# Optimization experiments

Measured on AMD Instinct MI355X. Metric: run time of the kernel, lower is better.

Reference implementation:

```python
import jax, jax.numpy as jnp
import numpy as np

BS, D, N, E, L, NE = 8, 512, 2048, 8, 64, 524288


def conv1d_same(x, w, b):
    # x: [B, W, Cin], w: [K, Cin, Cout] -> [B, W, Cout], stride 1, 'same' padding
    y = jax.lax.conv_general_dilated(x, w, window_strides=(1,), padding='SAME',
                                     dimension_numbers=('NWC', 'WIO', 'NWC'))
    return y + b


def setup_inputs() -> dict:
    key = jax.random.key(0)
    ks = jax.random.split(key, 10)
    def nrm(k, shape, s=1.0):
        return jax.random.normal(k, shape, jnp.float32) * s
    return {
        'latent': nrm(ks[0], (BS, D)),
        'edge_index': jax.random.randint(ks[1], (2, NE), 0, BS * N),
        'W_dense': nrm(ks[2], (D, N), 0.05),
        'b_dense': jnp.zeros((N,), jnp.float32),
        'conv1_w': nrm(ks[3], (3, 1, E), 0.3),
        'conv1_b': jnp.zeros((E,), jnp.float32),
        'gat_Wq': nrm(ks[4], (E, E), 0.3),
        'gat_bq': jnp.zeros((E,), jnp.float32),
        'gat_Wk': nrm(ks[5], (E, E), 0.3),
        'gat_bk': jnp.zeros((E,), jnp.float32),
        'gat_Wv': nrm(ks[6], (E, E), 0.3),
        'gat_bias': jnp.zeros((E,), jnp.float32),
        'qkv_w': nrm(ks[7], (3, E, 3 * E * L), 0.1),
        'qkv_b': jnp.zeros((3 * E * L,), jnp.float32),
    }


def reference(latent, edge_index, W_dense, b_dense, conv1_w, conv1_b,
              gat_Wq, gat_bq, gat_Wk, gat_bk, gat_Wv, gat_bias, qkv_w, qkv_b):
    bs = latent.shape[0]
    # Dense -> [bs, N], expand -> Conv1D(E) -> [bs, N, E]
    skeleton = latent @ W_dense + b_dense
    skeleton = conv1d_same(skeleton[..., None], conv1_w, conv1_b)
    # concat(unstack, axis=0) == reshape to batched graph nodes [bs*N, E]
    x = skeleton.reshape(bs * N, E)
    BN = bs * N
    # GAT (tf_geometric, num_heads=1): add self-loops, per-edge dot-attention,
    # segment softmax over destination (row), scatter-sum aggregate.
    loops = jnp.arange(BN)
    row = jnp.concatenate([edge_index[0], loops])
    col = jnp.concatenate([edge_index[1], loops])
    Q = jax.nn.leaky_relu(x @ gat_Wq + gat_bq, 0.2)
    K = jax.nn.leaky_relu(x @ gat_Wk + gat_bk, 0.2)
    V = x @ gat_Wv
    score = jnp.sum(Q[row] * K[col], axis=-1)            # [n_edges + BN]
    smax = jax.ops.segment_max(score, row, num_segments=BN)
    ex = jnp.exp(score - smax[row])
    ssum = jax.ops.segment_sum(ex, row, num_segments=BN)
    alpha = ex / ssum[row]                               # segment softmax
    h = jax.ops.segment_sum(alpha[:, None] * V[col], row, num_segments=BN) + gat_bias
    graph = h.reshape(bs, N, E)                          # stack(split(., bs))
    # QVK conv over node axis -> [bs, N, 3*E*L]
    qvk = conv1d_same(graph, qkv_w, qkv_b)
    # stack(split(., L, -1), 1) then concat(unstack(., -2), -1)
    qvk = qvk.reshape(bs, N, L, 3 * E).transpose(0, 2, 1, 3).reshape(bs, L, N * 3 * E)
    q, v, k = jnp.split(qvk, 3, axis=-1)                 # each [bs, L, N*E]
    # keras Attention (use_scale=False): softmax(q @ k^T) @ v
    attn = jax.nn.softmax(jnp.einsum('btd,bsd->bts', q, k), axis=-1)
    seq = jnp.einsum('bts,bsd->btd', attn, v)
    # stack(split(., N, -1), -2) == reshape [bs, L, N, E]
    return seq.reshape(bs, L, N, E)
```

## Files before the change

kernel.cpp:

```cpp
#include <hip/hip_runtime.h>
#include <hip/hip_bf16.h>
#include <math.h>

#define BSZ 8
#define DDIM 512
#define NND 2048
#define EE 8
#define LLH 64
#define NEDGE 524288
#define BNN 16384
#define OCC 1536
#define DQ 16384

typedef __attribute__((ext_vector_type(8))) short short8;
typedef __attribute__((ext_vector_type(4))) unsigned short ushort4v;

__device__ inline unsigned short f2bf(float x) {
    __hip_bfloat16 h = __float2bfloat16(x);
    return __builtin_bit_cast(unsigned short, h);
}
__device__ inline float bf2f(unsigned short u) {
    return __uint_as_float(((unsigned int)u) << 16);
}

__global__ __launch_bounds__(256) void k_densep(const float* __restrict__ latent,
                                                const float* __restrict__ Wd,
                                                const float* __restrict__ qw,
                                                const float* __restrict__ qb,
                                                float* __restrict__ pdense,
                                                int* __restrict__ hist,
                                                float* __restrict__ BsT) {
    int n0 = blockIdx.x * 32, d0 = blockIdx.y * 64;
    __shared__ float lat[8][64];
    int tid = threadIdx.x;
    if (blockIdx.y == 0) hist[blockIdx.x * 256 + tid] = 0;
    if (blockIdx.y == 1) {
        for (int idx = blockIdx.x * 256 + tid; idx < 38400; idx += 16384) {
            int jc = idx >> 6, s = idx & 63;
            int j = jc / 24, c = jc - j * 24;
            int sc = (c < 16) ? c + 8 : c - 16;
            BsT[idx] = (j < 24) ? qw[(size_t)j * OCC + s * 24 + sc] : qb[s * 24 + sc];
        }
    }
    #pragma unroll
    for (int r = 0; r < 2; ++r) {
        int i = r * 256 + tid;
        lat[i >> 6][i & 63] = latent[(i >> 6) * DDIM + d0 + (i & 63)];
    }
    __syncthreads();
    int nl = tid & 31, b = tid >> 5;
    const float* wp = Wd + (size_t)d0 * NND + n0 + nl;
    float acc = 0.f;
    #pragma unroll 8
    for (int d = 0; d < 64; ++d) acc += lat[b][d] * wp[(size_t)d * NND];
    pdense[((size_t)blockIdx.y * BSZ + b) * NND + n0 + nl] = acc;
}

__global__ __launch_bounds__(256) void k_gat(const float* __restrict__ pdense,
                                             const float* __restrict__ bd,
                                             const float* __restrict__ w1,
                                             const float* __restrict__ b1,
                                             const float* __restrict__ Wq, const float* __restrict__ bq,
                                             const float* __restrict__ Wk, const float* __restrict__ bk,
                                             const float* __restrict__ Wv,
                                             const int* __restrict__ ei,
                                             float* __restrict__ Qg, float* __restrict__ Kg,
                                             float* __restrict__ Vg, int* __restrict__ hist) {
    int gid = blockIdx.x * 256 + threadIdx.x;
    int i = gid >> 3, j = gid & 7;
    int b = i >> 11, n = i & (NND - 1);
    float sm = 0.f, s0 = 0.f, sp = 0.f;
    #pragma unroll
    for (int ds = 0; ds < 8; ++ds) {
        const float* p = pdense + ((size_t)ds * BSZ + b) * NND + n;
        if (n > 0) sm += p[-1];
        s0 += p[0];
        if (n < NND - 1) sp += p[1];
    }
    if (n > 0) sm += bd[n - 1];
    s0 += bd[n];
    if (n < NND - 1) sp += bd[n + 1];
    float q = bq[j], k = bk[j], v = 0.f;
    #pragma unroll
    for (int c = 0; c < EE; ++c) {
        float xc = sm * w1[c] + s0 * w1[EE + c] + sp * w1[2 * EE + c] + b1[c];
        q += xc * Wq[c * EE + j];
        k += xc * Wk[c * EE + j];
        v += xc * Wv[c * EE + j];
    }
    Qg[(size_t)i * EE + j] = (q >= 0.f) ? q : 0.2f * q;
    Kg[(size_t)i * EE + j] = (k >= 0.f) ? k : 0.2f * k;
    Vg[(size_t)i * EE + j] = v;
    #pragma unroll
    for (int r = 0; r < 4; ++r)
        atomicAdd(hist + ei[gid + r * 131072], 1);
}

__global__ __launch_bounds__(1024) void k_scan(const int* __restrict__ hist,
                                               int* __restrict__ offs,
                                               int* __restrict__ cnt) {
    int tid = threadIdx.x;
    int lane = tid & 63, wv = tid >> 6;
    const int4* hp = (const int4*)(hist + tid * 16);
    int4 a = hp[0], b4 = hp[1], c4 = hp[2], d4 = hp[3];
    int h[16] = {a.x, a.y, a.z, a.w, b4.x, b4.y, b4.z, b4.w,
                 c4.x, c4.y, c4.z, c4.w, d4.x, d4.y, d4.z, d4.w};
    int mysum = 0;
    #pragma unroll
    for (int i = 0; i < 16; ++i) mysum += h[i];
    int inc = mysum;
    #pragma unroll
    for (int off = 1; off < 64; off <<= 1) {
        int u = __shfl_up(inc, off, 64);
        if (lane >= off) inc += u;
    }
    __shared__ int wtot[16];
    if (lane == 63) wtot[wv] = inc;
    __syncthreads();
    if (tid < 16) {
        int t = wtot[tid];
        #pragma unroll
        for (int off = 1; off < 16; off <<= 1) {
            int u = __shfl_up(t, off, 16);
            if (tid >= off) t += u;
        }
        wtot[tid] = t;
    }
    __syncthreads();
    int run = (wv ? wtot[wv - 1] : 0) + inc - mysum;
    #pragma unroll
    for (int i = 0; i < 16; ++i) {
        offs[tid * 16 + i] = run;
        cnt[tid * 16 + i] = run;
        run += h[i];
    }
}

__global__ void k_scatter(const int* __restrict__ ei, int* __restrict__ cnt,
                          int* __restrict__ ecol) {
    int e = blockIdx.x * 256 + threadIdx.x;
    if (e >= NEDGE) return;
    int r = ei[e], c = ei[NEDGE + e];
    int pos = atomicAdd(cnt + r, 1);
    ecol[pos] = c;
}

__global__ __launch_bounds__(256) void k_gatagg(const int* __restrict__ ecol,
                                                const int* __restrict__ offs,
                                                const int* __restrict__ hist,
                                                const float* __restrict__ Qg,
                                                const float* __restrict__ Kg,
                                                const float* __restrict__ Vg,
                                                const float* __restrict__ gbias,
                                                float* __restrict__ hg) {
    int row = __builtin_amdgcn_readfirstlane(blockIdx.x * 4 + (threadIdx.x >> 6));
    int lane = threadIdx.x & 63;
    const float* Qr = Qg + (size_t)row * EE;
    float q0 = Qr[0], q1 = Qr[1], q2 = Qr[2], q3 = Qr[3];
    float q4 = Qr[4], q5 = Qr[5], q6 = Qr[6], q7 = Qr[7];
    int beg = offs[row], deg = hist[row];
    int total = deg + 1;
    float m = -INFINITY, l = 0.f;
    float acc[EE];
    #pragma unroll
    for (int j = 0; j < EE; ++j) acc[j] = 0.f;
    for (int base = 0; base < total; base += 64) {
        int idx = base + lane;
        int c = row;
        if (idx < deg) c = ecol[beg + idx];
        const float4* K4 = (const float4*)(Kg + (size_t)c * EE);
        float4 ka = K4[0], kb = K4[1];
        float s = q0*ka.x + q1*ka.y + q2*ka.z + q3*ka.w
                + q4*kb.x + q5*kb.y + q6*kb.z + q7*kb.w;
        if (idx >= total) s = -INFINITY;
        float pm = s;
        #pragma unroll
        for (int off = 32; off > 0; off >>= 1) pm = fmaxf(pm, __shfl_xor(pm, off));
        float nm = fmaxf(m, pm);
        float scale = __expf(m - nm);
        float p = (idx < total) ? __expf(s - nm) : 0.f;
        float ps = p;
        #pragma unroll
        for (int off = 32; off > 0; off >>= 1) ps += __shfl_xor(ps, off);
        l = l * scale + ps;
        const float4* V4 = (const float4*)(Vg + (size_t)c * EE);
        float4 va = V4[0], vb = V4[1];
        float pv[EE] = {p*va.x, p*va.y, p*va.z, p*va.w, p*vb.x, p*vb.y, p*vb.z, p*vb.w};
        #pragma unroll
        for (int j = 0; j < EE; ++j) {
            float t = pv[j];
            #pragma unroll
            for (int off = 32; off > 0; off >>= 1) t += __shfl_xor(t, off);
            acc[j] = acc[j] * scale + t;
        }
        m = nm;
    }
    if (lane < EE)
        hg[(size_t)row * EE + lane] = acc[lane] / l + gbias[lane];
}

__global__ __launch_bounds__(256) void k_convV(const float* __restrict__ hg,
                                               const float* __restrict__ qw,
                                               const float* __restrict__ qb,
                                               unsigned short* __restrict__ FvT,
                                               float* __restrict__ Mpart) {
    int bx = blockIdx.x, b = blockIdx.y, tid = threadIdx.x;
    if (bx < 86) {
        int n0 = 682 + bx * 8;
        __shared__ float hs[10 * EE];
        __shared__ unsigned short st[8 * 768];
        for (int i = tid; i < 10 * EE; i += 256) {
            int nn = n0 - 1 + (i >> 3);
            hs[i] = (nn < NND) ? hg[((size_t)b * NND + nn) * EE + (i & 7)] : 0.f;
        }
        __syncthreads();
        int dbase = n0 * 24 - DQ;
        #pragma unroll
        for (int pass = 0; pass < 2; ++pass) {
            if (pass) __syncthreads();
            float w[3][24], bias[3];
            #pragma unroll
            for (int rr = 0; rr < 3; ++rr) {
                int o = pass * 768 + rr * 256 + tid;
                bias[rr] = qb[o];
                #pragma unroll
                for (int kk = 0; kk < 24; ++kk) w[rr][kk] = qw[kk * OCC + o];
            }
            #pragma unroll
            for (int nn = 0; nn < 8; ++nn) {
                const float* hv = &hs[nn * EE];
                float a0 = bias[0], a1 = bias[1], a2 = bias[2];
                #pragma unroll
                for (int kk = 0; kk < 24; ++kk) {
                    float h = hv[kk];
                    a0 += h * w[0][kk]; a1 += h * w[1][kk]; a2 += h * w[2][kk];
                }
                st[nn * 768 + tid]       = f2bf(a0);
                st[nn * 768 + tid + 256] = f2bf(a1);
                st[nn * 768 + tid + 512] = f2bf(a2);
            }
            __syncthreads();
            int l0 = pass * 32;
            #pragma unroll
            for (int it = 0; it < 6; ++it) {
                int idx = it * 256 + tid;
                int dl = idx >> 3, s4 = idx & 7;
                int d = dbase + dl;
                if (d < 0 || d >= DQ) continue;
                int nn = dl / 24, c = dl - nn * 24;
                const unsigned short* sb = st + nn * 768 + c;
                ushort4v v4 = { sb[(s4 * 4 + 0) * 24], sb[(s4 * 4 + 1) * 24],
                                sb[(s4 * 4 + 2) * 24], sb[(s4 * 4 + 3) * 24] };
                *(ushort4v*)(FvT + ((size_t)b * DQ + d) * 64 + l0 + s4 * 4) = v4;
            }
        }
    } else {
        int sp = bx - 86;
        int nq0 = sp * 86;
        __shared__ float hq[88 * EE];
        __shared__ float hk[90 * EE];
        for (int i = tid; i < 88 * EE; i += 256) {
            int r = nq0 - 1 + (i >> 3);
            hq[i] = (r >= 0 && r < NND) ? hg[((size_t)b * NND + r) * EE + (i & 7)] : 0.f;
        }
        for (int i = tid; i < 90 * EE; i += 256) {
            int r = nq0 + 1364 + (i >> 3);
            hk[i] = (r < NND) ? hg[((size_t)b * NND + r) * EE + (i & 7)] : 0.f;
        }
        __syncthreads();
        int cnt1 = 683 - nq0; if (cnt1 > 86) cnt1 = 86; if (cnt1 < 0) cnt1 = 0;
        int cnt2 = 682 - nq0; if (cnt2 > 86) cnt2 = 86; if (cnt2 < 0) cnt2 = 0;
        for (int idx = tid; idx < 1250; idx += 256) {
            int mm = idx / 625, p = idx - (idx / 625) * 625;
            int i = p / 25, j = p - (p / 25) * 25;
            int cnt = mm ? cnt2 : cnt1;
            int qi = i >> 3, qe = i & 7;
            int kj = (j >> 3) + mm, ke = j & 7;
            float acc = 0.f;
            if (i < 24 && j < 24) {
                for (int nl = 0; nl < cnt; ++nl)
                    acc += hq[(nl + qi) * EE + qe] * hk[(nl + kj) * EE + ke];
            } else if (i < 24) {
                for (int nl = 0; nl < cnt; ++nl) acc += hq[(nl + qi) * EE + qe];
            } else if (j < 24) {
                for (int nl = 0; nl < cnt; ++nl) acc += hk[(nl + kj) * EE + ke];
            } else {
                acc = (float)cnt;
            }
            Mpart[((size_t)(sp * 8 + b)) * 1250 + idx] = acc;
        }
    }
}

__global__ __launch_bounds__(256) void k_Ssm(const float* __restrict__ qw,
                                             const float* __restrict__ qb,
                                             const float* __restrict__ Mpart,
                                             const float* __restrict__ BsT,
                                             float* __restrict__ atT) {
    int t = blockIdx.x, b = blockIdx.y, tid = threadIdx.x;
    __shared__ float Ms[1250];
    __shared__ float As[600];
    __shared__ float T1[600];
    __shared__ float part[4][64];
    for (int idx = tid; idx < 1250; idx += 256) {
        float s = 0.f;
        #pragma unroll
        for (int sp = 0; sp < 8; ++sp)
            s += Mpart[((size_t)(sp * 8 + b)) * 1250 + idx];
        Ms[idx] = s;
    }
    for (int idx = tid; idx < 600; idx += 256) {
        int i = idx / 24, c = idx - (idx / 24) * 24;
        As[idx] = (i < 24) ? qw[(size_t)i * OCC + t * 24 + c] : qb[t * 24 + c];
    }
    __syncthreads();
    for (int idx = tid; idx < 600; idx += 256) {
        int j = idx / 24, c = idx - (idx / 24) * 24;
        int mo = (c < 16) ? 0 : 625;
        float acc = 0.f;
        #pragma unroll 5
        for (int i = 0; i < 25; ++i)
            acc += Ms[mo + i * 25 + j] * As[i * 24 + c];
        T1[idx] = acc;
    }
    __syncthreads();
    int s = tid & 63, g = tid >> 6;
    float acc = 0.f;
    const float* bp = BsT + (size_t)(g * 150) * 64 + s;
    #pragma unroll 10
    for (int u = 0; u < 150; ++u)
        acc += T1[g * 150 + u] * bp[(size_t)u * 64];
    part[g][s] = acc;
    __syncthreads();
    if (tid < 64) {
        float v = part[0][s] + part[1][s] + part[2][s] + part[3][s];
        float m = v;
        #pragma unroll
        for (int off = 32; off > 0; off >>= 1) m = fmaxf(m, __shfl_xor(m, off));
        float e = __expf(v - m);
        float sum = e;
        #pragma unroll
        for (int off = 32; off > 0; off >>= 1) sum += __shfl_xor(sum, off);
        atT[((size_t)b * LLH + s) * LLH + t] = e / sum;
    }
}

__global__ __launch_bounds__(256) void k_attnV(const unsigned short* __restrict__ FvT,
                                               const float* __restrict__ atT,
                                               float* __restrict__ out) {
    int b = blockIdx.y;
    int d0 = blockIdx.x * 64;
    int tid = threadIdx.x;
    __shared__ float vtf[64][65];
    #pragma unroll
    for (int r = 0; r < 2; ++r) {
        int idx = r * 256 + tid;
        int dl = idx >> 3, g = idx & 7;
        short8 v = *(const short8*)(FvT + ((size_t)b * DQ + d0 + dl) * 64 + g * 8);
        #pragma unroll
        for (int j = 0; j < 8; ++j)
            vtf[dl][g * 8 + j] = bf2f((unsigned short)v[j]);
    }
    __syncthreads();
    int lane = tid & 63;
    int t0 = __builtin_amdgcn_readfirstlane((tid >> 6) * 16);
    const float* arow = atT + (size_t)b * LLH * LLH + t0;
    float acc[16];
    #pragma unroll
    for (int tt = 0; tt < 16; ++tt) acc[tt] = 0.f;
    #pragma unroll 4
    for (int s = 0; s < LLH; ++s) {
        float vv = vtf[lane][s];
        #pragma unroll
        for (int tt = 0; tt < 16; ++tt)
            acc[tt] += arow[s * LLH + tt] * vv;
    }
    float* ob = out + ((size_t)b * LLH + t0) * DQ + d0 + lane;
    #pragma unroll
    for (int tt = 0; tt < 16; ++tt) ob[(size_t)tt * DQ] = acc[tt];
}

extern "C" void kernel_launch(void* const* d_in, const int* in_sizes, int n_in,
                              void* d_out, int out_size, void* d_ws, size_t ws_size,
                              hipStream_t stream) {
    (void)in_sizes; (void)n_in; (void)out_size; (void)ws_size;
    const float* latent = (const float*)d_in[0];
    const int*   ei     = (const int*)d_in[1];
    const float* Wd     = (const float*)d_in[2];
    const float* bd     = (const float*)d_in[3];
    const float* w1     = (const float*)d_in[4];
    const float* b1     = (const float*)d_in[5];
    const float* Wq     = (const float*)d_in[6];
    const float* bq     = (const float*)d_in[7];
    const float* Wk     = (const float*)d_in[8];
    const float* bk     = (const float*)d_in[9];
    const float* Wv     = (const float*)d_in[10];
    const float* gbias  = (const float*)d_in[11];
    const float* qw     = (const float*)d_in[12];
    const float* qb     = (const float*)d_in[13];
    float* out = (float*)d_out;

    float* ws     = (float*)d_ws;
    float* pdense = ws;
    float* Qg     = pdense + 64 * NND;
    float* Kg     = Qg + BNN * EE;
    float* Vg     = Kg + BNN * EE;
    float* hg     = Vg + BNN * EE;
    int*   hist   = (int*)(hg + BNN * EE);
    int*   offs   = hist + BNN;
    int*   cnt    = offs + BNN;
    int*   ecol   = cnt + BNN;
    float* Mp     = (float*)(ecol + NEDGE);
    float* BsT    = Mp + 80000;
    float* atT    = BsT + 38400;
    unsigned short* FvT = (unsigned short*)(atT + BSZ * LLH * LLH);

    k_densep<<<dim3(64, 8), dim3(256), 0, stream>>>(latent, Wd, qw, qb, pdense, hist, BsT);
    k_gat<<<dim3(512), dim3(256), 0, stream>>>(pdense, bd, w1, b1, Wq, bq, Wk, bk, Wv,
                                               ei, Qg, Kg, Vg, hist);
    k_scan<<<dim3(1), dim3(1024), 0, stream>>>(hist, offs, cnt);
    k_scatter<<<dim3(NEDGE / 256), dim3(256), 0, stream>>>(ei, cnt, ecol);
    k_gatagg<<<dim3(BNN / 4), dim3(256), 0, stream>>>(ecol, offs, hist,
                                                      Qg, Kg, Vg, gbias, hg);
    k_convV<<<dim3(94, 8), dim3(256), 0, stream>>>(hg, qw, qb, FvT, Mp);
    k_Ssm<<<dim3(64, 8), dim3(256), 0, stream>>>(qw, qb, Mp, BsT, atT);
    k_attnV<<<dim3(256, 8), dim3(256), 0, stream>>>(FvT, atT, out);
}
```

Before: 134.9 us.

## Merge GAT build, scan, scatter and conv/softmax stages using software grid barriers

Fuses the GAT projection, histogram scan and edge scatter into one kernel separated by atomic-counter grid barriers, and likewise fuses the conv/V kernel with the attention-score softmax kernel. The aim is to remove kernel launch gaps and idle tails between small dependent stages (eight launches become five). It relies on all 512 or 752 blocks being co-resident for the spin barriers to avoid deadlock. It also serializes the scan into a single block while the other blocks spin.

```diff
diff --git a/kernel.cpp b/kernel.cpp
--- a/kernel.cpp
+++ b/kernel.cpp
@@ -23,17 +23,32 @@
     return __uint_as_float(((unsigned int)u) << 16);
 }
 
+__device__ inline void gridbar(int* c, int target) {
+    __syncthreads();
+    if (threadIdx.x == 0) {
+        __threadfence();
+        atomicAdd(c, 1);
+        while (atomicAdd(c, 0) < target) __builtin_amdgcn_s_sleep(8);
+        __threadfence();
+    }
+    __syncthreads();
+}
+
 __global__ __launch_bounds__(256) void k_densep(const float* __restrict__ latent,
                                                 const float* __restrict__ Wd,
                                                 const float* __restrict__ qw,
                                                 const float* __restrict__ qb,
                                                 float* __restrict__ pdense,
                                                 int* __restrict__ hist,
-                                                float* __restrict__ BsT) {
+                                                float* __restrict__ BsT,
+                                                int* __restrict__ cbar) {
     int n0 = blockIdx.x * 32, d0 = blockIdx.y * 64;
     __shared__ float lat[8][64];
     int tid = threadIdx.x;
-    if (blockIdx.y == 0) hist[blockIdx.x * 256 + tid] = 0;
+    if (blockIdx.y == 0) {
+        hist[blockIdx.x * 256 + tid] = 0;
+        if (blockIdx.x == 0 && tid < 16) cbar[tid] = 0;
+    }
     if (blockIdx.y == 1) {
         for (int idx = blockIdx.x * 256 + tid; idx < 38400; idx += 16384) {
             int jc = idx >> 6, s = idx & 63;
@@ -56,93 +71,85 @@
     pdense[((size_t)blockIdx.y * BSZ + b) * NND + n0 + nl] = acc;
 }
 
-__global__ __launch_bounds__(256) void k_gat(const float* __restrict__ pdense,
-                                             const float* __restrict__ bd,
-                                             const float* __restrict__ w1,
-                                             const float* __restrict__ b1,
-                                             const float* __restrict__ Wq, const float* __restrict__ bq,
-                                             const float* __restrict__ Wk, const float* __restrict__ bk,
-                                             const float* __restrict__ Wv,
-                                             const int* __restrict__ ei,
-                                             float* __restrict__ Qg, float* __restrict__ Kg,
-                                             float* __restrict__ Vg, int* __restrict__ hist) {
-    int gid = blockIdx.x * 256 + threadIdx.x;
-    int i = gid >> 3, j = gid & 7;
-    int b = i >> 11, n = i & (NND - 1);
-    float sm = 0.f, s0 = 0.f, sp = 0.f;
-    #pragma unroll
-    for (int ds = 0; ds < 8; ++ds) {
-        const float* p = pdense + ((size_t)ds * BSZ + b) * NND + n;
-        if (n > 0) sm += p[-1];
-        s0 += p[0];
-        if (n < NND - 1) sp += p[1];
-    }
-    if (n > 0) sm += bd[n - 1];
-    s0 += bd[n];
-    if (n < NND - 1) sp += bd[n + 1];
-    float q = bq[j], k = bk[j], v = 0.f;
-    #pragma unroll
-    for (int c = 0; c < EE; ++c) {
-        float xc = sm * w1[c] + s0 * w1[EE + c] + sp * w1[2 * EE + c] + b1[c];
-        q += xc * Wq[c * EE + j];
-        k += xc * Wk[c * EE + j];
-        v += xc * Wv[c * EE + j];
-    }
-    Qg[(size_t)i * EE + j] = (q >= 0.f) ? q : 0.2f * q;
-    Kg[(size_t)i * EE + j] = (k >= 0.f) ? k : 0.2f * k;
-    Vg[(size_t)i * EE + j] = v;
-    #pragma unroll
-    for (int r = 0; r < 4; ++r)
-        atomicAdd(hist + ei[gid + r * 131072], 1);
-}
-
-__global__ __launch_bounds__(1024) void k_scan(const int* __restrict__ hist,
-                                               int* __restrict__ offs,
-                                               int* __restrict__ cnt) {
+__global__ __launch_bounds__(256) void k_gatFull(const float* __restrict__ pdense,
+                                                 const float* __restrict__ bd,
+                                                 const float* __restrict__ w1,
+                                                 const float* __restrict__ b1,
+                                                 const float* __restrict__ Wq, const float* __restrict__ bq,
+                                                 const float* __restrict__ Wk, const float* __restrict__ bk,
+                                                 const float* __restrict__ Wv,
+                                                 const int* __restrict__ ei,
+                                                 float* __restrict__ Qg, float* __restrict__ Kg,
+                                                 float* __restrict__ Vg, int* __restrict__ hist,
+                                                 int* __restrict__ offs, int* __restrict__ cnt,
+                                                 int* __restrict__ ecol, int* __restrict__ cbar) {
     int tid = threadIdx.x;
-    int lane = tid & 63, wv = tid >> 6;
-    const int4* hp = (const int4*)(hist + tid * 16);
-    int4 a = hp[0], b4 = hp[1], c4 = hp[2], d4 = hp[3];
-    int h[16] = {a.x, a.y, a.z, a.w, b4.x, b4.y, b4.z, b4.w,
-                 c4.x, c4.y, c4.z, c4.w, d4.x, d4.y, d4.z, d4.w};
-    int mysum = 0;
-    #pragma unroll
-    for (int i = 0; i < 16; ++i) mysum += h[i];
-    int inc = mysum;
-    #pragma unroll
-    for (int off = 1; off < 64; off <<= 1) {
-        int u = __shfl_up(inc, off, 64);
-        if (lane >= off) inc += u;
-    }
-    __shared__ int wtot[16];
-    if (lane == 63) wtot[wv] = inc;
-    __syncthreads();
-    if (tid < 16) {
-        int t = wtot[tid];
-        #pragma unroll
-        for (int off = 1; off < 16; off <<= 1) {
-            int u = __shfl_up(t, off, 16);
-            if (tid >= off) t += u;
-        }
-        wtot[tid] = t;
-    }
-    __syncthreads();
-    int run = (wv ? wtot[wv - 1] : 0) + inc - mysum;
-    #pragma unroll
-    for (int i = 0; i < 16; ++i) {
-        offs[tid * 16 + i] = run;
-        cnt[tid * 16 + i] = run;
-        run += h[i];
-    }
-}
-
-__global__ void k_scatter(const int* __restrict__ ei, int* __restrict__ cnt,
-                          int* __restrict__ ecol) {
-    int e = blockIdx.x * 256 + threadIdx.x;
-    if (e >= NEDGE) return;
-    int r = ei[e], c = ei[NEDGE + e];
-    int pos = atomicAdd(cnt + r, 1);
-    ecol[pos] = c;
+    int gid = blockIdx.x * 256 + tid;
+    {
+        int i = gid >> 3, j = gid & 7;
+        int b = i >> 11, n = i & (NND - 1);
+        float sm = 0.f, s0 = 0.f, sp = 0.f;
+        #pragma unroll
+        for (int ds = 0; ds < 8; ++ds) {
+            const float* p = pdense + ((size_t)ds * BSZ + b) * NND + n;
+            if (n > 0) sm += p[-1];
+            s0 += p[0];
+            if (n < NND - 1) sp += p[1];
+        }
+        if (n > 0) sm += bd[n - 1];
+        s0 += bd[n];
+        if (n < NND - 1) sp += bd[n + 1];
+        float q = bq[j], k = bk[j], v = 0.f;
+        #pragma unroll
+        for (int c = 0; c < EE; ++c) {
+            float xc = sm * w1[c] + s0 * w1[EE + c] + sp * w1[2 * EE + c] + b1[c];
+            q += xc * Wq[c * EE + j];
+            k += xc * Wk[c * EE + j];
+            v += xc * Wv[c * EE + j];
+        }
+        Qg[(size_t)i * EE + j] = (q >= 0.f) ? q : 0.2f * q;
+        Kg[(size_t)i * EE + j] = (k >= 0.f) ? k : 0.2f * k;
+        Vg[(size_t)i * EE + j] = v;
+        #pragma unroll
+        for (int r = 0; r < 4; ++r)
+            atomicAdd(hist + ei[gid + r * 131072], 1);
+    }
+    gridbar(cbar + 0, 512);
+    if (blockIdx.x == 0) {
+        __shared__ int part[256];
+        int base = tid * 64;
+        const int4* h4 = (const int4*)(hist + base);
+        int sum = 0;
+        #pragma unroll
+        for (int i = 0; i < 16; ++i) { int4 v = h4[i]; sum += v.x + v.y + v.z + v.w; }
+        part[tid] = sum;
+        __syncthreads();
+        for (int off = 1; off < 256; off <<= 1) {
+            int v = (tid >= off) ? part[tid - off] : 0;
+            __syncthreads();
+            part[tid] += v;
+            __syncthreads();
+        }
+        int run = (tid > 0) ? part[tid - 1] : 0;
+        #pragma unroll
+        for (int i = 0; i < 16; ++i) {
+            int4 v = h4[i];
+            offs[base + i*4 + 0] = run; cnt[base + i*4 + 0] = run; run += v.x;
+            offs[base + i*4 + 1] = run; cnt[base + i*4 + 1] = run; run += v.y;
+            offs[base + i*4 + 2] = run; cnt[base + i*4 + 2] = run; run += v.z;
+            offs[base + i*4 + 3] = run; cnt[base + i*4 + 3] = run; run += v.w;
+        }
+    }
+    gridbar(cbar + 1, 512);
+    {
+        #pragma unroll
+        for (int r = 0; r < 4; ++r) {
+            int e = gid + r * 131072;
+            int rr = ei[e], c = ei[NEDGE + e];
+            int pos = atomicAdd(cnt + rr, 1);
+            ecol[pos] = c;
+        }
+    }
 }
 
 __global__ __launch_bounds__(256) void k_gatagg(const int* __restrict__ ecol,
@@ -199,16 +206,21 @@
         hg[(size_t)row * EE + lane] = acc[lane] / l + gbias[lane];
 }
 
-__global__ __launch_bounds__(256) void k_convV(const float* __restrict__ hg,
-                                               const float* __restrict__ qw,
-                                               const float* __restrict__ qb,
-                                               unsigned short* __restrict__ FvT,
-                                               float* __restrict__ Mpart) {
+__global__ __launch_bounds__(256) void k_convSsm(const float* __restrict__ hg,
+                                                 const float* __restrict__ qw,
+                                                 const float* __restrict__ qb,
+                                                 const float* __restrict__ Mpart_w,
+                                                 const float* __restrict__ BsT,
+                                                 unsigned short* __restrict__ FvT,
+                                                 float* __restrict__ Mpart,
+                                                 float* __restrict__ atT,
+                                                 int* __restrict__ cbar) {
+    __shared__ float smem[3456];
     int bx = blockIdx.x, b = blockIdx.y, tid = threadIdx.x;
     if (bx < 86) {
         int n0 = 682 + bx * 8;
-        __shared__ float hs[10 * EE];
-        __shared__ unsigned short st[8 * 768];
+        float* hs = smem;
+        unsigned short* st = (unsigned short*)(smem + 80);
         for (int i = tid; i < 10 * EE; i += 256) {
             int nn = n0 - 1 + (i >> 3);
             hs[i] = (nn < NND) ? hg[((size_t)b * NND + nn) * EE + (i & 7)] : 0.f;
@@ -257,8 +269,8 @@
     } else {
         int sp = bx - 86;
         int nq0 = sp * 86;
-        __shared__ float hq[88 * EE];
-        __shared__ float hk[90 * EE];
+        float* hq = smem;
+        float* hk = smem + 704;
         for (int i = tid; i < 88 * EE; i += 256) {
             int r = nq0 - 1 + (i >> 3);
             hq[i] = (r >= 0 && r < NND) ? hg[((size_t)b * NND + r) * EE + (i & 7)] : 0.f;
@@ -290,23 +302,20 @@
             Mpart[((size_t)(sp * 8 + b)) * 1250 + idx] = acc;
         }
     }
-}
-
-__global__ __launch_bounds__(256) void k_Ssm(const float* __restrict__ qw,
-                                             const float* __restrict__ qb,
-                                             const float* __restrict__ Mpart,
-                                             const float* __restrict__ BsT,
-                                             float* __restrict__ atT) {
-    int t = blockIdx.x, b = blockIdx.y, tid = threadIdx.x;
-    __shared__ float Ms[1250];
-    __shared__ float As[600];
-    __shared__ float T1[600];
-    __shared__ float part[4][64];
+    gridbar(cbar + 2, 752);
+    int fid = b * 94 + bx;
+    if (fid >= 512) return;
+    int t = fid >> 3, b2 = fid & 7;
+    float* Ms = smem;
+    float* As = smem + 1250;
+    float* T1 = smem + 1850;
+    float* part = smem + 2450;
+    __syncthreads();
     for (int idx = tid; idx < 1250; idx += 256) {
         float s = 0.f;
         #pragma unroll
         for (int sp = 0; sp < 8; ++sp)
-            s += Mpart[((size_t)(sp * 8 + b)) * 1250 + idx];
+            s += Mpart_w[((size_t)(sp * 8 + b2)) * 1250 + idx];
         Ms[idx] = s;
     }
     for (int idx = tid; idx < 600; idx += 256) {
@@ -330,10 +339,10 @@
     #pragma unroll 10
     for (int u = 0; u < 150; ++u)
         acc += T1[g * 150 + u] * bp[(size_t)u * 64];
-    part[g][s] = acc;
+    part[g * 64 + s] = acc;
     __syncthreads();
     if (tid < 64) {
-        float v = part[0][s] + part[1][s] + part[2][s] + part[3][s];
+        float v = part[s] + part[64 + s] + part[128 + s] + part[192 + s];
         float m = v;
         #pragma unroll
         for (int off = 32; off > 0; off >>= 1) m = fmaxf(m, __shfl_xor(m, off));
@@ -341,7 +350,7 @@
         float sum = e;
         #pragma unroll
         for (int off = 32; off > 0; off >>= 1) sum += __shfl_xor(sum, off);
-        atT[((size_t)b * LLH + s) * LLH + t] = e / sum;
+        atT[((size_t)b2 * LLH + s) * LLH + t] = e / sum;
     }
 }
 
@@ -410,19 +419,17 @@
     int*   offs   = hist + BNN;
     int*   cnt    = offs + BNN;
     int*   ecol   = cnt + BNN;
-    float* Mp     = (float*)(ecol + NEDGE);
+    int*   cbar   = ecol + NEDGE;
+    float* Mp     = (float*)(cbar + 16);
     float* BsT    = Mp + 80000;
     float* atT    = BsT + 38400;
     unsigned short* FvT = (unsigned short*)(atT + BSZ * LLH * LLH);
 
-    k_densep<<<dim3(64, 8), dim3(256), 0, stream>>>(latent, Wd, qw, qb, pdense, hist, BsT);
-    k_gat<<<dim3(512), dim3(256), 0, stream>>>(pdense, bd, w1, b1, Wq, bq, Wk, bk, Wv,
-                                               ei, Qg, Kg, Vg, hist);
-    k_scan<<<dim3(1), dim3(1024), 0, stream>>>(hist, offs, cnt);
-    k_scatter<<<dim3(NEDGE / 256), dim3(256), 0, stream>>>(ei, cnt, ecol);
+    k_densep<<<dim3(64, 8), dim3(256), 0, stream>>>(latent, Wd, qw, qb, pdense, hist, BsT, cbar);
+    k_gatFull<<<dim3(512), dim3(256), 0, stream>>>(pdense, bd, w1, b1, Wq, bq, Wk, bk, Wv,
+                                                   ei, Qg, Kg, Vg, hist, offs, cnt, ecol, cbar);
     k_gatagg<<<dim3(BNN / 4), dim3(256), 0, stream>>>(ecol, offs, hist,
                                                       Qg, Kg, Vg, gbias, hg);
-    k_convV<<<dim3(94, 8), dim3(256), 0, stream>>>(hg, qw, qb, FvT, Mp);
-    k_Ssm<<<dim3(64, 8), dim3(256), 0, stream>>>(qw, qb, Mp, BsT, atT);
+    k_convSsm<<<dim3(94, 8), dim3(256), 0, stream>>>(hg, qw, qb, Mp, BsT, FvT, Mp, atT, cbar);
     k_attnV<<<dim3(256, 8), dim3(256), 0, stream>>>(FvT, atT, out);
 }
```

Measured after the change: 291.7 us. 116% more time.
